# Kernel tuning notes

Hardware: AMD Instinct MI355X
Metric: run time of the kernel (lower is better)

The kernel has to match this reference:

```python
import jax, jax.numpy as jnp
import numpy as np

HEADS = 16
DIM_HEAD = 64
SCALE = DIM_HEAD ** -0.5


def setup_inputs() -> dict:
    key = jax.random.key(0)
    ks = jax.random.split(key, 5)
    b, n, dim = 2, 2048, 1024
    inner = HEADS * DIM_HEAD  # 1024
    std = dim ** -0.5
    return {
        "x": jax.random.normal(ks[0], (b, n, dim), jnp.float32),
        "ln_gamma": jnp.ones((dim,), jnp.float32),
        "ln_beta": jnp.zeros((dim,), jnp.float32),
        "W_qk": jax.random.normal(ks[1], (dim, 2 * inner), jnp.float32) * std,
        "W_v": jax.random.normal(ks[2], (dim, inner), jnp.float32) * std,
        "W_out": jax.random.normal(ks[3], (inner, dim), jnp.float32) * std,
        "b_out": jnp.zeros((dim,), jnp.float32),
    }


def _layernorm(x, gamma, beta, eps=1e-5):
    mu = jnp.mean(x, axis=-1, keepdims=True)
    var = jnp.var(x, axis=-1, keepdims=True)
    return (x - mu) * jax.lax.rsqrt(var + eps) * gamma + beta


def reference(x, ln_gamma, ln_beta, W_qk, W_v, W_out, b_out):
    b, n, dim = x.shape
    h, d = HEADS, DIM_HEAD
    xn = _layernorm(x, ln_gamma, ln_beta)
    qk = xn @ W_qk                      # [b, n, 2*h*d]
    q, k = jnp.split(qk, 2, axis=-1)    # each [b, n, h*d]
    v = xn @ W_v                        # [b, n, h*d]
    # b n (h d) -> b h n d
    q = q.reshape(b, n, h, d).transpose(0, 2, 1, 3)
    k = k.reshape(b, n, h, d).transpose(0, 2, 1, 3)
    v = v.reshape(b, n, h, d).transpose(0, 2, 1, 3)
    dots = jnp.einsum('bhid,bhjd->bhij', q, k) * SCALE
    attn = jax.nn.softmax(dots, axis=-1)
    out = jnp.einsum('bhij,bhjd->bhid', attn, v)
    out = out.transpose(0, 2, 1, 3).reshape(b, n, h * d)
    return out @ W_out + b_out
```

## Files before the change

### kernel.cpp

```cpp
#include <hip/hip_runtime.h>

#define HEADS 16
#define DHEAD 64
#define BATCH 2
#define SEQ   2048
#define DIM   1024
#define ROWS  (BATCH*SEQ)
#define SCALE_LOG2E 0.180336880f

typedef short v8s __attribute__((ext_vector_type(8)));
typedef float v4f __attribute__((ext_vector_type(4)));

__device__ __forceinline__ float fast_exp2(float x) {
    return __builtin_amdgcn_exp2f(x);
}

__device__ __forceinline__ unsigned short f2bf(float f) {
    unsigned u = __float_as_uint(f);
    u += 0x7FFFu + ((u >> 16) & 1u);
    return (unsigned short)(u >> 16);
}

__device__ __forceinline__ unsigned pk_bf2(float hi, float lo) {
    return __builtin_amdgcn_perm(__float_as_uint(hi), __float_as_uint(lo), 0x07060302u);
}

#define GLDS16(g, l) __builtin_amdgcn_global_load_lds( \
    (__attribute__((address_space(1))) void*)(g), \
    (__attribute__((address_space(3))) void*)(l), 16, 0, 0)

__global__ __launch_bounds__(256) void ln_kernel(const float* __restrict__ x,
                                                 const float* __restrict__ gamma,
                                                 const float* __restrict__ beta,
                                                 unsigned short* __restrict__ xn) {
    int row = blockIdx.x;
    const float* xr = x + (size_t)row * DIM;
    int t = threadIdx.x;
    float4 v = *(const float4*)(xr + t * 4);
    float s  = v.x + v.y + v.z + v.w;
    float sq = v.x * v.x + v.y * v.y + v.z * v.z + v.w * v.w;
#pragma unroll
    for (int off = 32; off > 0; off >>= 1) {
        s  += __shfl_down(s,  off, 64);
        sq += __shfl_down(sq, off, 64);
    }
    __shared__ float ss[4], ssq[4];
    int wave = t >> 6, lane = t & 63;
    if (lane == 0) { ss[wave] = s; ssq[wave] = sq; }
    __syncthreads();
    float tot  = ss[0] + ss[1] + ss[2] + ss[3];
    float totq = ssq[0] + ssq[1] + ssq[2] + ssq[3];
    float mean = tot * (1.f / DIM);
    float var  = totq * (1.f / DIM) - mean * mean;
    float rstd = rsqrtf(var + 1e-5f);
    float4 g = *(const float4*)(gamma + t * 4);
    float4 bb = *(const float4*)(beta + t * 4);
    ushort4 o;
    o.x = f2bf((v.x - mean) * rstd * g.x + bb.x);
    o.y = f2bf((v.y - mean) * rstd * g.y + bb.y);
    o.z = f2bf((v.z - mean) * rstd * g.z + bb.z);
    o.w = f2bf((v.w - mean) * rstd * g.w + bb.w);
    *(ushort4*)(xn + (size_t)row * DIM + t * 4) = o;
}

__global__ __launch_bounds__(256) void tr_all_kernel(const float* __restrict__ Wqk,
                                                     const float* __restrict__ Wv,
                                                     const float* __restrict__ Wout,
                                                     unsigned short* __restrict__ Tqk,
                                                     unsigned short* __restrict__ Tv,
                                                     unsigned short* __restrict__ To) {
    int z = blockIdx.z;
    const float* W = (z == 0) ? Wqk : (z == 1) ? Wv : Wout;
    unsigned short* Wt = (z == 0) ? Tqk : (z == 1) ? Tv : To;
    int Nw = (z == 0) ? 2048 : 1024;
    int n0 = blockIdx.x * 64, k0 = blockIdx.y * 64;
    if (n0 >= Nw) return;
    __shared__ float tile[64][65];
    int tid = threadIdx.x;
#pragma unroll
    for (int l = 0; l < 4; ++l) {
        int kk = (tid >> 4) + l * 16;
        int nn = (tid & 15) * 4;
        float4 v = *(const float4*)(W + (size_t)(k0 + kk) * Nw + n0 + nn);
        tile[kk][nn + 0] = v.x; tile[kk][nn + 1] = v.y;
        tile[kk][nn + 2] = v.z; tile[kk][nn + 3] = v.w;
    }
    __syncthreads();
#pragma unroll
    for (int l = 0; l < 4; ++l) {
        int cid = tid + l * 256;
        int nn = cid >> 4, kc = (cid & 15) * 4;
        ushort4 o;
        o.x = f2bf(tile[kc + 0][nn]);
        o.y = f2bf(tile[kc + 1][nn]);
        o.z = f2bf(tile[kc + 2][nn]);
        o.w = f2bf(tile[kc + 3][nn]);
        *(ushort4*)(Wt + (size_t)(n0 + nn) * DIM + k0 + kc) = o;
    }
}

template<int BN, bool SWAP>
__device__ __forceinline__ void mm_core2(const unsigned short* __restrict__ A,
                                         const unsigned short* __restrict__ Bt,
                                         int K, int aTile, int bTile,
                                         unsigned short (*As)[32],
                                         unsigned short (*Bs)[32],
                                         v4f (*acc)[4]) {
    constexpr int MI = (BN == 128) ? 4 : 2;
    int t = threadIdx.x;
    int w = t >> 6, L = t & 63, l15 = L & 15, quad = L >> 4;
    int aOff = (BN == 128) ? (w >> 1) * 64 : w * 32;
    int bOff = (BN == 128) ? (w & 1) * 64 : 0;
    int srow = L >> 2, schunk = (L & 3) * 8;
    for (int k0 = 0; k0 < K; k0 += 32) {
        __syncthreads();
#pragma unroll
        for (int j = 0; j < 2; ++j) {
            int g = w * 2 + j;
            GLDS16(A + (size_t)(aTile + g * 16 + srow) * K + k0 + schunk,
                   &As[g * 16][0]);
        }
#pragma unroll
        for (int j = 0; j < BN / 64; ++j) {
            int g = (BN == 128) ? (w * 2 + j) : w;
            GLDS16(Bt + (size_t)(bTile + g * 16 + srow) * K + k0 + schunk,
                   &Bs[g * 16][0]);
        }
        __syncthreads();
        v8s a[MI], b[4];
#pragma unroll
        for (int i = 0; i < MI; ++i) a[i] = *(const v8s*)&As[aOff + i * 16 + l15][quad * 8];
#pragma unroll
        for (int j = 0; j < 4; ++j) b[j] = *(const v8s*)&Bs[bOff + j * 16 + l15][quad * 8];
#pragma unroll
        for (int i = 0; i < MI; ++i)
#pragma unroll
            for (int j = 0; j < 4; ++j)
                acc[i][j] = SWAP
                    ? __builtin_amdgcn_mfma_f32_16x16x32_bf16(b[j], a[i], acc[i][j], 0, 0, 0)
                    : __builtin_amdgcn_mfma_f32_16x16x32_bf16(a[i], b[j], acc[i][j], 0, 0, 0);
    }
}

__global__ __launch_bounds__(256) void gemm_qkv_kernel(const unsigned short* __restrict__ A,
                                                       const unsigned short* __restrict__ Bt,
                                                       unsigned short* __restrict__ q_h,
                                                       unsigned short* __restrict__ k_h,
                                                       unsigned short* __restrict__ v_t) {
    __shared__ __align__(16) unsigned short As[128][32];
    __shared__ __align__(16) unsigned short Bs[128][32];
    int t = threadIdx.x, w = t >> 6, L = t & 63, l15 = L & 15, quad = L >> 4;
    int aTile = blockIdx.y * 128, bTile = blockIdx.x * 128;
    int aOff = (w >> 1) * 64, bOff = (w & 1) * 64;
    v4f acc[4][4] = {};
    if (bTile < 2048) {
        mm_core2<128, true>(A, Bt, DIM, aTile, bTile, As, Bs, acc);
#pragma unroll
        for (int j = 0; j < 4; ++j) {
            int col = bTile + bOff + j * 16 + quad * 4;
            unsigned short* dst = (col < 1024) ? q_h : k_h;
            int c = col & 1023;
            int h = c >> 6, d = c & 63;
#pragma unroll
            for (int i = 0; i < 4; ++i) {
                int m = aTile + aOff + i * 16 + l15;
                int b = m >> 11, seq = m & 2047;
                ushort4 o;
                o.x = f2bf(acc[i][j][0]); o.y = f2bf(acc[i][j][1]);
                o.z = f2bf(acc[i][j][2]); o.w = f2bf(acc[i][j][3]);
                *(ushort4*)(dst + (((size_t)(b * 16 + h)) * SEQ + seq) * 64 + d) = o;
            }
        }
    } else {
        mm_core2<128, false>(A, Bt, DIM, aTile, bTile, As, Bs, acc);
#pragma unroll
        for (int j = 0; j < 4; ++j) {
            int c = bTile + bOff + j * 16 + l15 - 2048;
            int h = c >> 6, d = c & 63;
#pragma unroll
            for (int i = 0; i < 4; ++i) {
                int m0 = aTile + aOff + i * 16 + quad * 4;
                int b = m0 >> 11, seq0 = m0 & 2047;
                ushort4 o;
                o.x = f2bf(acc[i][j][0]); o.y = f2bf(acc[i][j][1]);
                o.z = f2bf(acc[i][j][2]); o.w = f2bf(acc[i][j][3]);
                *(ushort4*)(v_t + (((size_t)(b * 16 + h)) * 64 + d) * SEQ + seq0) = o;
            }
        }
    }
}

__global__ __launch_bounds__(256) void gemm_out_kernel(const unsigned short* __restrict__ A,
                                                       const unsigned short* __restrict__ Bt,
                                                       const float* __restrict__ bias,
                                                       float* __restrict__ C) {
    __shared__ __align__(16) unsigned short As[128][32];
    __shared__ __align__(16) unsigned short Bs[64][32];
    int t = threadIdx.x, w = t >> 6, L = t & 63, l15 = L & 15, quad = L >> 4;
    int aTile = blockIdx.y * 128, bTile = blockIdx.x * 64;
    v4f acc[2][4] = {};
    mm_core2<64, true>(A, Bt, DIM, aTile, bTile, As, Bs, acc);
#pragma unroll
    for (int j = 0; j < 4; ++j) {
        int n = bTile + j * 16 + quad * 4;
        float4 bv = *(const float4*)(bias + n);
#pragma unroll
        for (int i = 0; i < 2; ++i) {
            int m = aTile + w * 32 + i * 16 + l15;
            float4 o = make_float4(acc[i][j][0] + bv.x, acc[i][j][1] + bv.y,
                                   acc[i][j][2] + bv.z, acc[i][j][3] + bv.w);
            *(float4*)(C + (size_t)m * DIM + n) = o;
        }
    }
}

__global__ __launch_bounds__(256) void attn_kernel(const unsigned short* __restrict__ q_h,
                                                   const unsigned short* __restrict__ k_h,
                                                   const unsigned short* __restrict__ v_t,
                                                   unsigned short* __restrict__ ao) {
    __shared__ __align__(16) unsigned short KF[8 * 64 * 8];
    __shared__ __align__(16) unsigned short VF[8 * 64 * 8];
    __shared__ __align__(16) unsigned short Pld[4][2][16 * 72];
    int qt = blockIdx.x, h = blockIdx.y, b = blockIdx.z;
    int bh = b * HEADS + h;
    int w = threadIdx.x >> 6;
    int L = threadIdx.x & 63, l15 = L & 15, quad = L >> 4;

    const unsigned short* qp = q_h + ((size_t)bh * SEQ + qt * 128 + w * 32 + l15) * 64 + quad * 8;
    v8s qf[2][2];
    qf[0][0] = *(const v8s*)(qp);
    qf[0][1] = *(const v8s*)(qp + 32);
    qf[1][0] = *(const v8s*)(qp + 16 * 64);
    qf[1][1] = *(const v8s*)(qp + 16 * 64 + 32);

    const unsigned short* kstage = k_h + ((size_t)bh * SEQ + w * 16 + l15) * 64 + quad * 8;
    const unsigned short* vstage = v_t + ((size_t)bh * 64 + w * 16 + l15) * SEQ + quad * 8;

    v4f o[2][4] = {};
    v4f lacc[2] = {};
    const short ob = (short)0x3F80;
    const v8s ones = {ob, ob, ob, ob, ob, ob, ob, ob};

    v8s ks0 = *(const v8s*)(kstage);
    v8s ks1 = *(const v8s*)(kstage + 32);
    v8s vs0 = *(const v8s*)(vstage);
    v8s vs1 = *(const v8s*)(vstage + 32);

    for (int j0 = 0; j0 < SEQ; j0 += 64) {
        __syncthreads();
        *(v8s*)&KF[((w * 2 + 0) * 64 + L) * 8] = ks0;
        *(v8s*)&KF[((w * 2 + 1) * 64 + L) * 8] = ks1;
        *(v8s*)&VF[((w * 2 + 0) * 64 + L) * 8] = vs0;
        *(v8s*)&VF[((w * 2 + 1) * 64 + L) * 8] = vs1;
        __syncthreads();
        if (j0 + 64 < SEQ) {
            ks0 = *(const v8s*)(kstage + (size_t)(j0 + 64) * 64);
            ks1 = *(const v8s*)(kstage + (size_t)(j0 + 64) * 64 + 32);
            vs0 = *(const v8s*)(vstage + j0 + 64);
            vs1 = *(const v8s*)(vstage + j0 + 64 + 32);
        }
        v8s kf[4][2], vf[4][2];
#pragma unroll
        for (int jt = 0; jt < 4; ++jt) {
            kf[jt][0] = *(const v8s*)&KF[((jt * 2 + 0) * 64 + L) * 8];
            kf[jt][1] = *(const v8s*)&KF[((jt * 2 + 1) * 64 + L) * 8];
            vf[jt][0] = *(const v8s*)&VF[((jt * 2 + 0) * 64 + L) * 8];
            vf[jt][1] = *(const v8s*)&VF[((jt * 2 + 1) * 64 + L) * 8];
        }
        v4f s[2][4] = {};
#pragma unroll
        for (int m = 0; m < 2; ++m)
#pragma unroll
            for (int jt = 0; jt < 4; ++jt) {
                s[m][jt] = __builtin_amdgcn_mfma_f32_16x16x32_bf16(kf[jt][0], qf[m][0], s[m][jt], 0, 0, 0);
                s[m][jt] = __builtin_amdgcn_mfma_f32_16x16x32_bf16(kf[jt][1], qf[m][1], s[m][jt], 0, 0, 0);
            }
#pragma unroll
        for (int m = 0; m < 2; ++m)
#pragma unroll
            for (int jt = 0; jt < 4; ++jt) {
                float p0 = fast_exp2(s[m][jt][0] * SCALE_LOG2E);
                float p1 = fast_exp2(s[m][jt][1] * SCALE_LOG2E);
                float p2 = fast_exp2(s[m][jt][2] * SCALE_LOG2E);
                float p3 = fast_exp2(s[m][jt][3] * SCALE_LOG2E);
                uint2 pk;
                pk.x = pk_bf2(p1, p0);
                pk.y = pk_bf2(p3, p2);
                *(uint2*)&Pld[w][m][l15 * 72 + jt * 16 + quad * 4] = pk;
            }
#pragma unroll
        for (int m = 0; m < 2; ++m) {
            v8s pb0 = *(const v8s*)&Pld[w][m][l15 * 72 + quad * 8];
            v8s pb1 = *(const v8s*)&Pld[w][m][l15 * 72 + 32 + quad * 8];
#pragma unroll
            for (int dt = 0; dt < 4; ++dt) {
                o[m][dt] = __builtin_amdgcn_mfma_f32_16x16x32_bf16(vf[dt][0], pb0, o[m][dt], 0, 0, 0);
                o[m][dt] = __builtin_amdgcn_mfma_f32_16x16x32_bf16(vf[dt][1], pb1, o[m][dt], 0, 0, 0);
            }
            lacc[m] = __builtin_amdgcn_mfma_f32_16x16x32_bf16(ones, pb0, lacc[m], 0, 0, 0);
            lacc[m] = __builtin_amdgcn_mfma_f32_16x16x32_bf16(ones, pb1, lacc[m], 0, 0, 0);
        }
    }
#pragma unroll
    for (int m = 0; m < 2; ++m) {
        float inv = 1.f / lacc[m][0];
        int rowg = b * SEQ + qt * 128 + w * 32 + m * 16 + l15;
#pragma unroll
        for (int dt = 0; dt < 4; ++dt) {
            ushort4 ov;
            ov.x = f2bf(o[m][dt][0] * inv);
            ov.y = f2bf(o[m][dt][1] * inv);
            ov.z = f2bf(o[m][dt][2] * inv);
            ov.w = f2bf(o[m][dt][3] * inv);
            *(ushort4*)(ao + (size_t)rowg * DIM + h * 64 + dt * 16 + quad * 4) = ov;
        }
    }
}

extern "C" void kernel_launch(void* const* d_in, const int* in_sizes, int n_in,
                              void* d_out, int out_size, void* d_ws, size_t ws_size,
                              hipStream_t stream) {
    const float* x     = (const float*)d_in[0];
    const float* gamma = (const float*)d_in[1];
    const float* beta  = (const float*)d_in[2];
    const float* Wqk   = (const float*)d_in[3];
    const float* Wv    = (const float*)d_in[4];
    const float* Wout  = (const float*)d_in[5];
    const float* bout  = (const float*)d_in[6];
    float* out = (float*)d_out;

    unsigned short* ws = (unsigned short*)d_ws;
    unsigned short* xn    = ws;
    unsigned short* Wt_qk = xn + (size_t)ROWS * DIM;
    unsigned short* Wt_v  = Wt_qk + (size_t)2048 * DIM;
    unsigned short* Wt_o  = Wt_v + (size_t)DIM * DIM;
    unsigned short* q_h   = Wt_o + (size_t)DIM * DIM;
    unsigned short* k_h   = q_h + (size_t)ROWS * DIM;
    unsigned short* v_t   = k_h + (size_t)ROWS * DIM;
    unsigned short* ao    = v_t + (size_t)ROWS * DIM;

    ln_kernel<<<ROWS, 256, 0, stream>>>(x, gamma, beta, xn);
    tr_all_kernel<<<dim3(32, 16, 3), 256, 0, stream>>>(Wqk, Wv, Wout, Wt_qk, Wt_v, Wt_o);
    gemm_qkv_kernel<<<dim3(3072 / 128, ROWS / 128), 256, 0, stream>>>(xn, Wt_qk, q_h, k_h, v_t);
    attn_kernel<<<dim3(SEQ / 128, HEADS, BATCH), 256, 0, stream>>>(q_h, k_h, v_t, ao);
    gemm_out_kernel<<<dim3(DIM / 64, ROWS / 128), 256, 0, stream>>>(ao, Wt_o, bout, out);
}
```

Before: 194.9 us.

## Split attention over key halves, merge prep kernels, restructure GEMM LDS layout

Attention is split into two key-range halves, doubling the grid. Each half writes unnormalized partial outputs and row sums, and a new combine kernel adds and normalizes them. The layernorm and weight-transpose kernels are merged into one launch. The GEMM core now loads K=64 per iteration into a fragment-ordered LDS layout, which halves the barriers per K. The split adds an extra kernel launch, extra global traffic for the partials, and bf16 rounding of the unnormalized partial sums.

```diff
diff --git a/kernel.cpp b/kernel.cpp
--- a/kernel.cpp
+++ b/kernel.cpp
@@ -21,6 +21,10 @@
     return (unsigned short)(u >> 16);
 }
 
+__device__ __forceinline__ float bf2f(unsigned short u) {
+    return __uint_as_float(((unsigned)u) << 16);
+}
+
 __device__ __forceinline__ unsigned pk_bf2(float hi, float lo) {
     return __builtin_amdgcn_perm(__float_as_uint(hi), __float_as_uint(lo), 0x07060302u);
 }
@@ -29,58 +33,57 @@
     (__attribute__((address_space(1))) void*)(g), \
     (__attribute__((address_space(3))) void*)(l), 16, 0, 0)
 
-__global__ __launch_bounds__(256) void ln_kernel(const float* __restrict__ x,
-                                                 const float* __restrict__ gamma,
-                                                 const float* __restrict__ beta,
-                                                 unsigned short* __restrict__ xn) {
-    int row = blockIdx.x;
-    const float* xr = x + (size_t)row * DIM;
+__global__ __launch_bounds__(256) void prep_kernel(const float* __restrict__ x,
+                                                   const float* __restrict__ gamma,
+                                                   const float* __restrict__ beta,
+                                                   const float* __restrict__ Wqk,
+                                                   const float* __restrict__ Wv,
+                                                   const float* __restrict__ Wout,
+                                                   unsigned short* __restrict__ xn,
+                                                   unsigned short* __restrict__ Tqk,
+                                                   unsigned short* __restrict__ Tv,
+                                                   unsigned short* __restrict__ To) {
+    __shared__ float tile[64][65];
+    __shared__ float ss[4], ssq[4];
+    int gid = blockIdx.x;
     int t = threadIdx.x;
-    float4 v = *(const float4*)(xr + t * 4);
-    float s  = v.x + v.y + v.z + v.w;
-    float sq = v.x * v.x + v.y * v.y + v.z * v.z + v.w * v.w;
-#pragma unroll
-    for (int off = 32; off > 0; off >>= 1) {
-        s  += __shfl_down(s,  off, 64);
-        sq += __shfl_down(sq, off, 64);
-    }
-    __shared__ float ss[4], ssq[4];
-    int wave = t >> 6, lane = t & 63;
-    if (lane == 0) { ss[wave] = s; ssq[wave] = sq; }
-    __syncthreads();
-    float tot  = ss[0] + ss[1] + ss[2] + ss[3];
-    float totq = ssq[0] + ssq[1] + ssq[2] + ssq[3];
-    float mean = tot * (1.f / DIM);
-    float var  = totq * (1.f / DIM) - mean * mean;
-    float rstd = rsqrtf(var + 1e-5f);
-    float4 g = *(const float4*)(gamma + t * 4);
-    float4 bb = *(const float4*)(beta + t * 4);
-    ushort4 o;
-    o.x = f2bf((v.x - mean) * rstd * g.x + bb.x);
-    o.y = f2bf((v.y - mean) * rstd * g.y + bb.y);
-    o.z = f2bf((v.z - mean) * rstd * g.z + bb.z);
-    o.w = f2bf((v.w - mean) * rstd * g.w + bb.w);
-    *(ushort4*)(xn + (size_t)row * DIM + t * 4) = o;
-}
-
-__global__ __launch_bounds__(256) void tr_all_kernel(const float* __restrict__ Wqk,
-                                                     const float* __restrict__ Wv,
-                                                     const float* __restrict__ Wout,
-                                                     unsigned short* __restrict__ Tqk,
-                                                     unsigned short* __restrict__ Tv,
-                                                     unsigned short* __restrict__ To) {
-    int z = blockIdx.z;
-    const float* W = (z == 0) ? Wqk : (z == 1) ? Wv : Wout;
-    unsigned short* Wt = (z == 0) ? Tqk : (z == 1) ? Tv : To;
-    int Nw = (z == 0) ? 2048 : 1024;
-    int n0 = blockIdx.x * 64, k0 = blockIdx.y * 64;
-    if (n0 >= Nw) return;
-    __shared__ float tile[64][65];
-    int tid = threadIdx.x;
+    if (gid < ROWS) {
+        const float* xr = x + (size_t)gid * DIM;
+        float4 v = *(const float4*)(xr + t * 4);
+        float s  = v.x + v.y + v.z + v.w;
+        float sq = v.x * v.x + v.y * v.y + v.z * v.z + v.w * v.w;
+#pragma unroll
+        for (int off = 32; off > 0; off >>= 1) {
+            s  += __shfl_down(s,  off, 64);
+            sq += __shfl_down(sq, off, 64);
+        }
+        int wave = t >> 6, lane = t & 63;
+        if (lane == 0) { ss[wave] = s; ssq[wave] = sq; }
+        __syncthreads();
+        float tot  = ss[0] + ss[1] + ss[2] + ss[3];
+        float totq = ssq[0] + ssq[1] + ssq[2] + ssq[3];
+        float mean = tot * (1.f / DIM);
+        float var  = totq * (1.f / DIM) - mean * mean;
+        float rstd = rsqrtf(var + 1e-5f);
+        float4 g = *(const float4*)(gamma + t * 4);
+        float4 bb = *(const float4*)(beta + t * 4);
+        ushort4 o;
+        o.x = f2bf((v.x - mean) * rstd * g.x + bb.x);
+        o.y = f2bf((v.y - mean) * rstd * g.y + bb.y);
+        o.z = f2bf((v.z - mean) * rstd * g.z + bb.z);
+        o.w = f2bf((v.w - mean) * rstd * g.w + bb.w);
+        *(ushort4*)(xn + (size_t)gid * DIM + t * 4) = o;
+        return;
+    }
+    int g2 = gid - ROWS;
+    const float* W; unsigned short* Wt; int Nw, n0, k0;
+    if (g2 < 512)      { W = Wqk;  Wt = Tqk; Nw = 2048; n0 = (g2 & 31) * 64; k0 = (g2 >> 5) * 64; }
+    else if (g2 < 768) { int g3 = g2 - 512; W = Wv;  Wt = Tv; Nw = 1024; n0 = (g3 & 15) * 64; k0 = (g3 >> 4) * 64; }
+    else               { int g3 = g2 - 768; W = Wout; Wt = To; Nw = 1024; n0 = (g3 & 15) * 64; k0 = (g3 >> 4) * 64; }
 #pragma unroll
     for (int l = 0; l < 4; ++l) {
-        int kk = (tid >> 4) + l * 16;
-        int nn = (tid & 15) * 4;
+        int kk = (t >> 4) + l * 16;
+        int nn = (t & 15) * 4;
         float4 v = *(const float4*)(W + (size_t)(k0 + kk) * Nw + n0 + nn);
         tile[kk][nn + 0] = v.x; tile[kk][nn + 1] = v.y;
         tile[kk][nn + 2] = v.z; tile[kk][nn + 3] = v.w;
@@ -88,7 +91,7 @@
     __syncthreads();
 #pragma unroll
     for (int l = 0; l < 4; ++l) {
-        int cid = tid + l * 256;
+        int cid = t + l * 256;
         int nn = cid >> 4, kc = (cid & 15) * 4;
         ushort4 o;
         o.x = f2bf(tile[kc + 0][nn]);
@@ -100,45 +103,53 @@
 }
 
 template<int BN, bool SWAP>
-__device__ __forceinline__ void mm_core2(const unsigned short* __restrict__ A,
+__device__ __forceinline__ void mm_core3(const unsigned short* __restrict__ A,
                                          const unsigned short* __restrict__ Bt,
                                          int K, int aTile, int bTile,
-                                         unsigned short (*As)[32],
-                                         unsigned short (*Bs)[32],
+                                         unsigned short* As,
+                                         unsigned short* Bs,
                                          v4f (*acc)[4]) {
     constexpr int MI = (BN == 128) ? 4 : 2;
+    constexpr int BSLOT = (BN == 128) ? 4 : 2;
     int t = threadIdx.x;
     int w = t >> 6, L = t & 63, l15 = L & 15, quad = L >> 4;
-    int aOff = (BN == 128) ? (w >> 1) * 64 : w * 32;
-    int bOff = (BN == 128) ? (w & 1) * 64 : 0;
-    int srow = L >> 2, schunk = (L & 3) * 8;
-    for (int k0 = 0; k0 < K; k0 += 32) {
-        __syncthreads();
-#pragma unroll
-        for (int j = 0; j < 2; ++j) {
-            int g = w * 2 + j;
-            GLDS16(A + (size_t)(aTile + g * 16 + srow) * K + k0 + schunk,
-                   &As[g * 16][0]);
-        }
-#pragma unroll
-        for (int j = 0; j < BN / 64; ++j) {
-            int g = (BN == 128) ? (w * 2 + j) : w;
-            GLDS16(Bt + (size_t)(bTile + g * 16 + srow) * K + k0 + schunk,
-                   &Bs[g * 16][0]);
-        }
-        __syncthreads();
-        v8s a[MI], b[4];
-#pragma unroll
-        for (int i = 0; i < MI; ++i) a[i] = *(const v8s*)&As[aOff + i * 16 + l15][quad * 8];
-#pragma unroll
-        for (int j = 0; j < 4; ++j) b[j] = *(const v8s*)&Bs[bOff + j * 16 + l15][quad * 8];
-#pragma unroll
-        for (int i = 0; i < MI; ++i)
+    int aOffT = (BN == 128) ? (w >> 1) * 4 : w * 2;
+    int bOffT = 0;
+    if (BN == 128) bOffT = (w & 1) * 4;
+    for (int k0 = 0; k0 < K; k0 += 64) {
+        __syncthreads();
+#pragma unroll
+        for (int j = 0; j < 4; ++j) {
+            int slot = w * 4 + j;
+            int g = slot >> 1, kk = slot & 1;
+            GLDS16(A + (size_t)(aTile + g * 16 + l15) * K + k0 + kk * 32 + quad * 8,
+                   As + slot * 512);
+        }
+#pragma unroll
+        for (int j = 0; j < BSLOT; ++j) {
+            int slot = w * BSLOT + j;
+            int g = slot >> 1, kk = slot & 1;
+            GLDS16(Bt + (size_t)(bTile + g * 16 + l15) * K + k0 + kk * 32 + quad * 8,
+                   Bs + slot * 512);
+        }
+        __syncthreads();
+#pragma unroll
+        for (int kk = 0; kk < 2; ++kk) {
+            v8s a[MI], b[4];
+#pragma unroll
+            for (int i = 0; i < MI; ++i)
+                a[i] = *(const v8s*)(As + ((aOffT + i) * 2 + kk) * 512 + L * 8);
 #pragma unroll
             for (int j = 0; j < 4; ++j)
-                acc[i][j] = SWAP
-                    ? __builtin_amdgcn_mfma_f32_16x16x32_bf16(b[j], a[i], acc[i][j], 0, 0, 0)
-                    : __builtin_amdgcn_mfma_f32_16x16x32_bf16(a[i], b[j], acc[i][j], 0, 0, 0);
+                b[j] = *(const v8s*)(Bs + ((bOffT + j) * 2 + kk) * 512 + L * 8);
+#pragma unroll
+            for (int i = 0; i < MI; ++i)
+#pragma unroll
+                for (int j = 0; j < 4; ++j)
+                    acc[i][j] = SWAP
+                        ? __builtin_amdgcn_mfma_f32_16x16x32_bf16(b[j], a[i], acc[i][j], 0, 0, 0)
+                        : __builtin_amdgcn_mfma_f32_16x16x32_bf16(a[i], b[j], acc[i][j], 0, 0, 0);
+        }
     }
 }
 
@@ -147,14 +158,14 @@
                                                        unsigned short* __restrict__ q_h,
                                                        unsigned short* __restrict__ k_h,
                                                        unsigned short* __restrict__ v_t) {
-    __shared__ __align__(16) unsigned short As[128][32];
-    __shared__ __align__(16) unsigned short Bs[128][32];
+    __shared__ __align__(16) unsigned short As[16 * 512];
+    __shared__ __align__(16) unsigned short Bs[16 * 512];
     int t = threadIdx.x, w = t >> 6, L = t & 63, l15 = L & 15, quad = L >> 4;
     int aTile = blockIdx.y * 128, bTile = blockIdx.x * 128;
     int aOff = (w >> 1) * 64, bOff = (w & 1) * 64;
     v4f acc[4][4] = {};
     if (bTile < 2048) {
-        mm_core2<128, true>(A, Bt, DIM, aTile, bTile, As, Bs, acc);
+        mm_core3<128, true>(A, Bt, DIM, aTile, bTile, As, Bs, acc);
 #pragma unroll
         for (int j = 0; j < 4; ++j) {
             int col = bTile + bOff + j * 16 + quad * 4;
@@ -172,7 +183,7 @@
             }
         }
     } else {
-        mm_core2<128, false>(A, Bt, DIM, aTile, bTile, As, Bs, acc);
+        mm_core3<128, false>(A, Bt, DIM, aTile, bTile, As, Bs, acc);
 #pragma unroll
         for (int j = 0; j < 4; ++j) {
             int c = bTile + bOff + j * 16 + l15 - 2048;
@@ -194,12 +205,12 @@
                                                        const unsigned short* __restrict__ Bt,
                                                        const float* __restrict__ bias,
                                                        float* __restrict__ C) {
-    __shared__ __align__(16) unsigned short As[128][32];
-    __shared__ __align__(16) unsigned short Bs[64][32];
+    __shared__ __align__(16) unsigned short As[16 * 512];
+    __shared__ __align__(16) unsigned short Bs[8 * 512];
     int t = threadIdx.x, w = t >> 6, L = t & 63, l15 = L & 15, quad = L >> 4;
     int aTile = blockIdx.y * 128, bTile = blockIdx.x * 64;
     v4f acc[2][4] = {};
-    mm_core2<64, true>(A, Bt, DIM, aTile, bTile, As, Bs, acc);
+    mm_core3<64, true>(A, Bt, DIM, aTile, bTile, As, Bs, acc);
 #pragma unroll
     for (int j = 0; j < 4; ++j) {
         int n = bTile + j * 16 + quad * 4;
@@ -217,11 +228,13 @@
 __global__ __launch_bounds__(256) void attn_kernel(const unsigned short* __restrict__ q_h,
                                                    const unsigned short* __restrict__ k_h,
                                                    const unsigned short* __restrict__ v_t,
-                                                   unsigned short* __restrict__ ao) {
+                                                   unsigned short* __restrict__ opart,
+                                                   float* __restrict__ lpart) {
     __shared__ __align__(16) unsigned short KF[8 * 64 * 8];
     __shared__ __align__(16) unsigned short VF[8 * 64 * 8];
     __shared__ __align__(16) unsigned short Pld[4][2][16 * 72];
-    int qt = blockIdx.x, h = blockIdx.y, b = blockIdx.z;
+    int qt = blockIdx.x >> 1, kh = blockIdx.x & 1;
+    int h = blockIdx.y, b = blockIdx.z;
     int bh = b * HEADS + h;
     int w = threadIdx.x >> 6;
     int L = threadIdx.x & 63, l15 = L & 15, quad = L >> 4;
@@ -241,19 +254,21 @@
     const short ob = (short)0x3F80;
     const v8s ones = {ob, ob, ob, ob, ob, ob, ob, ob};
 
-    v8s ks0 = *(const v8s*)(kstage);
-    v8s ks1 = *(const v8s*)(kstage + 32);
-    v8s vs0 = *(const v8s*)(vstage);
-    v8s vs1 = *(const v8s*)(vstage + 32);
-
-    for (int j0 = 0; j0 < SEQ; j0 += 64) {
+    int jbase = kh * 1024;
+    v8s ks0 = *(const v8s*)(kstage + (size_t)jbase * 64);
+    v8s ks1 = *(const v8s*)(kstage + (size_t)jbase * 64 + 32);
+    v8s vs0 = *(const v8s*)(vstage + jbase);
+    v8s vs1 = *(const v8s*)(vstage + jbase + 32);
+
+    for (int jj = 0; jj < 1024; jj += 64) {
+        int j0 = jbase + jj;
         __syncthreads();
         *(v8s*)&KF[((w * 2 + 0) * 64 + L) * 8] = ks0;
         *(v8s*)&KF[((w * 2 + 1) * 64 + L) * 8] = ks1;
         *(v8s*)&VF[((w * 2 + 0) * 64 + L) * 8] = vs0;
         *(v8s*)&VF[((w * 2 + 1) * 64 + L) * 8] = vs1;
         __syncthreads();
-        if (j0 + 64 < SEQ) {
+        if (jj + 64 < 1024) {
             ks0 = *(const v8s*)(kstage + (size_t)(j0 + 64) * 64);
             ks1 = *(const v8s*)(kstage + (size_t)(j0 + 64) * 64 + 32);
             vs0 = *(const v8s*)(vstage + j0 + 64);
@@ -303,18 +318,39 @@
     }
 #pragma unroll
     for (int m = 0; m < 2; ++m) {
-        float inv = 1.f / lacc[m][0];
-        int rowg = b * SEQ + qt * 128 + w * 32 + m * 16 + l15;
+        int seq = qt * 128 + w * 32 + m * 16 + l15;
+        int rowg = b * SEQ + seq;
+        if (quad == 0)
+            lpart[((size_t)(kh * 32 + bh)) * SEQ + seq] = lacc[m][0];
 #pragma unroll
         for (int dt = 0; dt < 4; ++dt) {
-            ushort4 ov;
-            ov.x = f2bf(o[m][dt][0] * inv);
-            ov.y = f2bf(o[m][dt][1] * inv);
-            ov.z = f2bf(o[m][dt][2] * inv);
-            ov.w = f2bf(o[m][dt][3] * inv);
-            *(ushort4*)(ao + (size_t)rowg * DIM + h * 64 + dt * 16 + quad * 4) = ov;
-        }
-    }
+            uint2 ov;
+            ov.x = pk_bf2(o[m][dt][1], o[m][dt][0]);
+            ov.y = pk_bf2(o[m][dt][3], o[m][dt][2]);
+            *(uint2*)(opart + ((size_t)kh * ROWS + rowg) * DIM + h * 64 + dt * 16 + quad * 4) = ov;
+        }
+    }
+}
+
+__global__ __launch_bounds__(256) void combine_kernel(const unsigned short* __restrict__ opart,
+                                                      const float* __restrict__ lpart,
+                                                      unsigned short* __restrict__ ao) {
+    int rowg = blockIdx.x, t = threadIdx.x;
+    int b = rowg >> 11, seq = rowg & 2047;
+    int h = t >> 4;
+    int bh = b * 16 + h;
+    float l0 = lpart[(size_t)bh * SEQ + seq];
+    float l1 = lpart[((size_t)(32 + bh)) * SEQ + seq];
+    float inv = 1.f / (l0 + l1);
+    size_t base = (size_t)rowg * DIM + t * 4;
+    ushort4 a0 = *(const ushort4*)(opart + base);
+    ushort4 a1 = *(const ushort4*)(opart + (size_t)ROWS * DIM + base);
+    ushort4 o;
+    o.x = f2bf((bf2f(a0.x) + bf2f(a1.x)) * inv);
+    o.y = f2bf((bf2f(a0.y) + bf2f(a1.y)) * inv);
+    o.z = f2bf((bf2f(a0.z) + bf2f(a1.z)) * inv);
+    o.w = f2bf((bf2f(a0.w) + bf2f(a1.w)) * inv);
+    *(ushort4*)(ao + base) = o;
 }
 
 extern "C" void kernel_launch(void* const* d_in, const int* in_sizes, int n_in,
@@ -338,10 +374,13 @@
     unsigned short* k_h   = q_h + (size_t)ROWS * DIM;
     unsigned short* v_t   = k_h + (size_t)ROWS * DIM;
     unsigned short* ao    = v_t + (size_t)ROWS * DIM;
-
-    ln_kernel<<<ROWS, 256, 0, stream>>>(x, gamma, beta, xn);
-    tr_all_kernel<<<dim3(32, 16, 3), 256, 0, stream>>>(Wqk, Wv, Wout, Wt_qk, Wt_v, Wt_o);
+    unsigned short* opart = ao + (size_t)ROWS * DIM;
+    float*          lpart = (float*)(opart + (size_t)2 * ROWS * DIM);
+
+    prep_kernel<<<ROWS + 1024, 256, 0, stream>>>(x, gamma, beta, Wqk, Wv, Wout,
+                                                 xn, Wt_qk, Wt_v, Wt_o);
     gemm_qkv_kernel<<<dim3(3072 / 128, ROWS / 128), 256, 0, stream>>>(xn, Wt_qk, q_h, k_h, v_t);
-    attn_kernel<<<dim3(SEQ / 128, HEADS, BATCH), 256, 0, stream>>>(q_h, k_h, v_t, ao);
+    attn_kernel<<<dim3(2 * SEQ / 128, HEADS, BATCH), 256, 0, stream>>>(q_h, k_h, v_t, opart, lpart);
+    combine_kernel<<<ROWS, 256, 0, stream>>>(opart, lpart, ao);
     gemm_out_kernel<<<dim3(DIM / 64, ROWS / 128), 256, 0, stream>>>(ao, Wt_o, bout, out);
 }
```

Result: slower. 230.0 us (+18.0%).
